# Kernel tuning notes

Measured on AMD Instinct MI355X. Metric: run time of the kernel, lower is better.

The kernel has to match this reference:

```python
import jax, jax.numpy as jnp
import numpy as np

# fp4 e2m1 positive value grid and midpoints between adjacent grid values
_GRID = jnp.array([0.0, 0.5, 1.0, 1.5, 2.0, 3.0, 4.0, 6.0], dtype=jnp.float32)
_MIDS = jnp.array([0.25, 0.75, 1.25, 1.75, 2.5, 3.5, 5.0], dtype=jnp.float32)
BLOCK = 32               # MX block size
E8M0_BIAS = 127
F32_MIN_NORMAL = float(2.0 ** -126)
F4_E2M1_MAX_POW2 = 2     # log2 of largest power-of-two <= 6.0 -> 4.0


def _quantize_fp4(a):
    """Round-to-nearest-even onto the signed e2m1 grid."""
    mag = jnp.clip(jnp.abs(a), 0.0, 6.0)
    idx = jnp.searchsorted(_MIDS, mag, side='left')  # ties round down
    mids_pad = jnp.concatenate([_MIDS, jnp.array([-1.0], jnp.float32)])
    tie = mag == mids_pad[idx]
    idx = jnp.where(tie & (idx % 2 == 1), idx + 1, idx)  # ties-to-even mantissa
    return _GRID[idx] * jnp.where(a < 0, -1.0, 1.0)


def _floor_log2(m):
    """Exact floor(log2(m)) for m > 0, with corrections for fp rounding of log2."""
    e = jnp.floor(jnp.log2(m))
    e = jnp.where(jnp.exp2(e) > m, e - 1.0, e)
    e = jnp.where(jnp.exp2(e + 1.0) <= m, e + 1.0, e)
    return e


def _qdq_mxfp4(x):
    """Quantize-dequantize x to MX fp4_e2m1, block 32, FLOOR scale mode (to_mx + to_dtype)."""
    shp = x.shape
    xb = x.reshape(-1, BLOCK)
    max_abs = jnp.max(jnp.abs(xb), axis=1)
    eps = F32_MIN_NORMAL * (max_abs == 0).astype(jnp.float32)
    pow2 = _floor_log2(max_abs + eps)
    e_unb = jnp.clip(pow2 - F4_E2M1_MAX_POW2, -float(E8M0_BIAS), float(E8M0_BIAS) + 1.0)
    scale = jnp.maximum(jnp.exp2(e_unb), F32_MIN_NORMAL)  # [nblk]
    q = _quantize_fp4(xb / scale[:, None])
    return (q * scale[:, None]).reshape(shp)


def _dequant_weight(weight_packed, weight_scale, out_f, in_f):
    """Unpack uint8-packed fp4 (low nibble first), apply e8m0 block scales."""
    p = weight_packed.astype(jnp.int32)
    low = p & 0xF
    high = (p >> 4) & 0xF
    nib = jnp.stack([low, high], axis=-1).reshape(out_f, in_f)  # interleave low,high
    vals = _GRID[nib & 7] * jnp.where((nib & 8) > 0, -1.0, 1.0)
    s = jnp.exp2(weight_scale.astype(jnp.float32) - E8M0_BIAS)  # get_fp_scale(e8m0)
    return (vals.reshape(-1, BLOCK) * s[:, None]).reshape(out_f, in_f)


def setup_inputs() -> dict:
    key = jax.random.key(0)
    k1, k2, k3 = jax.random.split(key, 3)
    M, IN, OUT = 4096, 4096, 4096
    x = jax.random.normal(k1, (M, IN), dtype=jnp.float32)
    weight_packed = jax.random.randint(k2, (OUT, IN // 2), 0, 256, dtype=jnp.int32)
    weight_scale = jax.random.randint(k3, (OUT * IN // BLOCK,), 0, 135, dtype=jnp.int32)
    return {"x": x, "weight_packed": weight_packed, "weight_scale": weight_scale}


def reference(x, weight_packed, weight_scale):
    out_f = weight_packed.shape[0]
    in_f = weight_packed.shape[1] * 2
    xq = _qdq_mxfp4(x)                                       # qdq_mxfp4(x)
    w_dq = _dequant_weight(weight_packed, weight_scale, out_f, in_f)
    return xq @ w_dq.T                                       # matmul(x, w_dq.t())
```

## Files before the change

kernel.cpp:

```cpp
#include <hip/hip_runtime.h>
#include <stdint.h>

typedef __attribute__((ext_vector_type(4)))  int   intx4;
typedef __attribute__((ext_vector_type(8)))  int   intx8;
typedef __attribute__((ext_vector_type(16))) float floatx16;

#define GLL16(gp, lp)                                                               \
    __builtin_amdgcn_global_load_lds((const __attribute__((address_space(1))) unsigned int*)(gp), \
                                     (__attribute__((address_space(3))) unsigned int*)(lp), 16, 0, 0)
#define GLL4(gp, lp)                                                                \
    __builtin_amdgcn_global_load_lds((const __attribute__((address_space(1))) unsigned int*)(gp), \
                                     (__attribute__((address_space(3))) unsigned int*)(lp), 4, 0, 0)

__device__ __forceinline__ uint32_t enc1(float xv, float inv) {
    float a = fminf(fabsf(xv) * inv, 6.0f);
    int e;
    if (a < 2.0f)      e = (int)rintf(a + a);
    else if (a < 4.0f) e = (int)rintf(a) + 2;
    else               e = (int)rintf(a * 0.5f) + 4;
    return (uint32_t)e | ((__float_as_uint(xv) >> 28) & 8u);
}

__global__ __launch_bounds__(256) void quant_x_kernel(const float* __restrict__ x,
                                                      uint32_t* __restrict__ xq,
                                                      uint8_t* __restrict__ xs_t,
                                                      int M, int K) {
    int t = blockIdx.x * 256 + threadIdx.x;
    int kbpr = K >> 5;
    int m = t / kbpr;
    int kb = t - m * kbpr;
    const float4* src = (const float4*)(x + (size_t)m * K + (size_t)kb * 32);
    float4 v[8];
#pragma unroll
    for (int i = 0; i < 8; ++i) v[i] = src[i];
    float mx = 0.f;
#pragma unroll
    for (int i = 0; i < 8; ++i)
        mx = fmaxf(mx, fmaxf(fmaxf(fabsf(v[i].x), fabsf(v[i].y)),
                             fmaxf(fabsf(v[i].z), fabsf(v[i].w))));
    unsigned ef = __float_as_uint(mx) >> 23;
    unsigned code = (ef < 3u) ? 1u : (ef - 2u);
    float inv = __uint_as_float((254u - code) << 23);

    uint32_t w[4];
#pragma unroll
    for (int d = 0; d < 4; ++d) {
        float4 va = v[2 * d], vb = v[2 * d + 1];
        w[d] =  enc1(va.x, inv)        | (enc1(va.y, inv) << 4)
             | (enc1(va.z, inv) << 8)  | (enc1(va.w, inv) << 12)
             | (enc1(vb.x, inv) << 16) | (enc1(vb.y, inv) << 20)
             | (enc1(vb.z, inv) << 24) | (enc1(vb.w, inv) << 28);
    }
    ((uint4*)xq)[t] = make_uint4(w[0], w[1], w[2], w[3]);
    xs_t[(size_t)kb * M + m] = (uint8_t)code;
}

__global__ __launch_bounds__(256) void tscale_kernel(const int* __restrict__ wsc,
                                                     uint8_t* __restrict__ ws_t,
                                                     int N, int kbpr) {
    int t = blockIdx.x * 256 + threadIdx.x;
    int n = t / kbpr;
    int kb = t - n * kbpr;
    ws_t[(size_t)kb * N + n] = (uint8_t)wsc[t];
}

__global__ __launch_bounds__(256) void repack_w_kernel(const int* __restrict__ wp,
                                                       uint32_t* __restrict__ wrep,
                                                       int n4) {
    int t = blockIdx.x * 256 + threadIdx.x;
    if (t >= n4) return;
    int4 p = ((const int4*)wp)[t];
    wrep[t] = (uint32_t)(p.x & 0xFF) | ((uint32_t)(p.y & 0xFF) << 8)
            | ((uint32_t)(p.z & 0xFF) << 16) | ((uint32_t)(p.w & 0xFF) << 24);
}

__global__ __launch_bounds__(256) void gemm_mx_kernel(const uint8_t* __restrict__ Apk,
                                                      const uint8_t* __restrict__ Bpk,
                                                      const uint8_t* __restrict__ AsT,
                                                      const uint8_t* __restrict__ BsT,
                                                      float* __restrict__ C,
                                                      int M, int N, int K) {
    __shared__ __align__(16) uint8_t sA[8192];
    __shared__ __align__(16) uint8_t sB[8192];
    __shared__ __align__(16) uint8_t sAs[512];
    __shared__ __align__(16) uint8_t sBs[512];

    const int tid = threadIdx.x;
    const int bm0 = blockIdx.y << 7;
    const int bn0 = blockIdx.x << 7;
    const int wave = tid >> 6;
    const int lane = tid & 63;
    const int wm = (wave >> 1) << 6;
    const int wn = (wave & 1) << 6;
    const int row = lane & 31;
    const int h = lane >> 5;
    const int Kb = K >> 1;

    const int s0 = tid, s1 = tid + 256;
    const int r0 = s0 >> 2, p0 = (s0 & 3) ^ (r0 & 3);
    const int r1 = s1 >> 2, p1 = (s1 & 3) ^ (r1 & 3);
    const uint8_t* Ag0 = Apk + (size_t)(bm0 + r0) * Kb + p0 * 16;
    const uint8_t* Ag1 = Apk + (size_t)(bm0 + r1) * Kb + p1 * 16;
    const uint8_t* Bg0 = Bpk + (size_t)(bn0 + r0) * Kb + p0 * 16;
    const uint8_t* Bg1 = Bpk + (size_t)(bn0 + r1) * Kb + p1 * 16;

    const int st = tid & 127;
    const int sj = st >> 5, si = st & 31;
    const uint8_t* Sg = (tid < 128) ? (AsT + (size_t)sj * M + bm0 + si * 4)
                                    : (BsT + (size_t)sj * N + bn0 + si * 4);
    uint8_t* Sl = (tid < 128) ? (sAs + st * 4) : (sBs + st * 4);
    const size_t sAdv = (size_t)4 * (size_t)((tid < 128) ? M : N);

    floatx16 acc[2][2];
#pragma unroll
    for (int a = 0; a < 2; ++a)
#pragma unroll
        for (int b = 0; b < 2; ++b)
#pragma unroll
            for (int r = 0; r < 16; ++r) acc[a][b][r] = 0.f;

    const int nchunk = K >> 7;
    for (int c = 0; c < nchunk; ++c) {
        __syncthreads();
        const size_t koff = (size_t)c << 6;
        GLL16(Ag0 + koff, sA + s0 * 16);
        GLL16(Ag1 + koff, sA + s1 * 16);
        GLL16(Bg0 + koff, sB + s0 * 16);
        GLL16(Bg1 + koff, sB + s1 * 16);
        GLL4(Sg + (size_t)c * sAdv, Sl);
        __syncthreads();

#pragma unroll
        for (int s = 0; s < 2; ++s) {
            intx4 a4[2], b4[2];
            int sa[2], sb[2];
            const int kp = 2 * s + h;
#pragma unroll
            for (int mt = 0; mt < 2; ++mt) {
                const int lr = wm + mt * 32 + row;
                a4[mt] = *(const intx4*)(sA + lr * 64 + ((kp ^ (lr & 3)) << 4));
                sa[mt] = sAs[kp * 128 + lr];
            }
#pragma unroll
            for (int nt = 0; nt < 2; ++nt) {
                const int lr = wn + nt * 32 + row;
                b4[nt] = *(const intx4*)(sB + lr * 64 + ((kp ^ (lr & 3)) << 4));
                sb[nt] = sBs[kp * 128 + lr];
            }
#pragma unroll
            for (int mt = 0; mt < 2; ++mt)
#pragma unroll
                for (int nt = 0; nt < 2; ++nt) {
                    intx8 a8 = {a4[mt][0], a4[mt][1], a4[mt][2], a4[mt][3], 0, 0, 0, 0};
                    intx8 b8 = {b4[nt][0], b4[nt][1], b4[nt][2], b4[nt][3], 0, 0, 0, 0};
                    acc[mt][nt] = __builtin_amdgcn_mfma_scale_f32_32x32x64_f8f6f4(
                        a8, b8, acc[mt][nt], 4, 4, 0, sa[mt], 0, sb[nt]);
                }
        }
    }

#pragma unroll
    for (int mt = 0; mt < 2; ++mt)
#pragma unroll
        for (int nt = 0; nt < 2; ++nt) {
            const int col = bn0 + wn + nt * 32 + row;
#pragma unroll
            for (int g = 0; g < 4; ++g) {
                const int rw = bm0 + wm + mt * 32 + 8 * g + 4 * h;
#pragma unroll
                for (int q = 0; q < 4; ++q)
                    C[(size_t)(rw + q) * N + col] = acc[mt][nt][4 * g + q];
            }
        }
}

extern "C" void kernel_launch(void* const* d_in, const int* in_sizes, int n_in,
                              void* d_out, int out_size, void* d_ws, size_t ws_size,
                              hipStream_t stream) {
    const float* x = (const float*)d_in[0];
    const int* wp = (const int*)d_in[1];
    const int* wsc = (const int*)d_in[2];
    float* out = (float*)d_out;

    const int K = 4096;
    const int M = in_sizes[0] / K;
    const int N = (in_sizes[1] * 2) / K;
    const int kbpr = K / 32;
    const int npack = N * K / 2;

    uint32_t* xq   = (uint32_t*)d_ws;
    uint8_t*  xs   = (uint8_t*)d_ws + (size_t)M * K / 2;
    uint8_t*  wst  = xs + (size_t)M * kbpr;
    uint32_t* wrep = (uint32_t*)(wst + (size_t)N * kbpr);

    quant_x_kernel<<<(M * kbpr) / 256, 256, 0, stream>>>(x, xq, xs, M, K);
    tscale_kernel<<<(N * kbpr) / 256, 256, 0, stream>>>(wsc, wst, N, kbpr);
    repack_w_kernel<<<(npack / 4 + 255) / 256, 256, 0, stream>>>(wp, wrep, npack / 4);

    dim3 grid(N / 128, M / 128);
    gemm_mx_kernel<<<grid, 256, 0, stream>>>((const uint8_t*)xq, (const uint8_t*)wrep,
                                             xs, wst, out, M, N, K);
}
```

Baseline: 204.2 us.

## Double-buffer GEMM LDS loads, row-major scales, fuse weight prep kernels

The GEMM main loop now uses two LDS buffers: the next K-chunk is issued with global_load_lds while the current one is computed, and explicit vmcnt waits plus barriers replace the two __syncthreads per chunk. MFMA sections are wrapped in s_setprio. Scales are stored row-major so each thread loads four consecutive scale bytes as one word, which removes the transposing scale kernel. The weight repack and scale packing are fused into one launch, and x quantization is remapped to one float4 per thread with a shuffle-based block max, which gives coalesced small writes at the cost of more threads. Doubling LDS use may lower occupancy.

```diff
diff --git a/kernel.cpp b/kernel.cpp
--- a/kernel.cpp
+++ b/kernel.cpp
@@ -23,67 +23,50 @@
 
 __global__ __launch_bounds__(256) void quant_x_kernel(const float* __restrict__ x,
                                                       uint32_t* __restrict__ xq,
-                                                      uint8_t* __restrict__ xs_t,
-                                                      int M, int K) {
-    int t = blockIdx.x * 256 + threadIdx.x;
-    int kbpr = K >> 5;
-    int m = t / kbpr;
-    int kb = t - m * kbpr;
-    const float4* src = (const float4*)(x + (size_t)m * K + (size_t)kb * 32);
-    float4 v[8];
-#pragma unroll
-    for (int i = 0; i < 8; ++i) v[i] = src[i];
-    float mx = 0.f;
-#pragma unroll
-    for (int i = 0; i < 8; ++i)
-        mx = fmaxf(mx, fmaxf(fmaxf(fabsf(v[i].x), fabsf(v[i].y)),
-                             fmaxf(fabsf(v[i].z), fabsf(v[i].w))));
-    unsigned ef = __float_as_uint(mx) >> 23;
-    unsigned code = (ef < 3u) ? 1u : (ef - 2u);
-    float inv = __uint_as_float((254u - code) << 23);
-
-    uint32_t w[4];
-#pragma unroll
-    for (int d = 0; d < 4; ++d) {
-        float4 va = v[2 * d], vb = v[2 * d + 1];
-        w[d] =  enc1(va.x, inv)        | (enc1(va.y, inv) << 4)
-             | (enc1(va.z, inv) << 8)  | (enc1(va.w, inv) << 12)
-             | (enc1(vb.x, inv) << 16) | (enc1(vb.y, inv) << 20)
-             | (enc1(vb.z, inv) << 24) | (enc1(vb.w, inv) << 28);
+                                                      uint8_t* __restrict__ xs) {
+    const int gl = blockIdx.x * 256 + threadIdx.x;
+    const float4 v = ((const float4*)x)[gl];
+    float m = fmaxf(fmaxf(fabsf(v.x), fabsf(v.y)), fmaxf(fabsf(v.z), fabsf(v.w)));
+    m = fmaxf(m, __shfl_xor(m, 1));
+    m = fmaxf(m, __shfl_xor(m, 2));
+    m = fmaxf(m, __shfl_xor(m, 4));
+    const unsigned ef = __float_as_uint(m) >> 23;
+    const unsigned code = (ef < 3u) ? 1u : (ef - 2u);
+    const float inv = __uint_as_float((254u - code) << 23);
+    const uint32_t p = enc1(v.x, inv)        | (enc1(v.y, inv) << 4)
+                     | (enc1(v.z, inv) << 8) | (enc1(v.w, inv) << 12);
+    ((uint16_t*)xq)[gl] = (uint16_t)p;
+    if ((gl & 7) == 0) xs[gl >> 3] = (uint8_t)code;
+}
+
+__global__ __launch_bounds__(256) void repack_kernel(const int* __restrict__ wp,
+                                                     uint32_t* __restrict__ wrep,
+                                                     int n4w,
+                                                     const int* __restrict__ wsc,
+                                                     uint32_t* __restrict__ ws,
+                                                     int n4s) {
+    const int t = blockIdx.x * 256 + threadIdx.x;
+    if (t < n4w) {
+        const int4 p = ((const int4*)wp)[t];
+        wrep[t] = (uint32_t)(p.x & 0xFF) | ((uint32_t)(p.y & 0xFF) << 8)
+                | ((uint32_t)(p.z & 0xFF) << 16) | ((uint32_t)(p.w & 0xFF) << 24);
+    } else if (t - n4w < n4s) {
+        const int i = t - n4w;
+        const int4 p = ((const int4*)wsc)[i];
+        ws[i] = (uint32_t)(p.x & 0xFF) | ((uint32_t)(p.y & 0xFF) << 8)
+              | ((uint32_t)(p.z & 0xFF) << 16) | ((uint32_t)(p.w & 0xFF) << 24);
     }
-    ((uint4*)xq)[t] = make_uint4(w[0], w[1], w[2], w[3]);
-    xs_t[(size_t)kb * M + m] = (uint8_t)code;
-}
-
-__global__ __launch_bounds__(256) void tscale_kernel(const int* __restrict__ wsc,
-                                                     uint8_t* __restrict__ ws_t,
-                                                     int N, int kbpr) {
-    int t = blockIdx.x * 256 + threadIdx.x;
-    int n = t / kbpr;
-    int kb = t - n * kbpr;
-    ws_t[(size_t)kb * N + n] = (uint8_t)wsc[t];
-}
-
-__global__ __launch_bounds__(256) void repack_w_kernel(const int* __restrict__ wp,
-                                                       uint32_t* __restrict__ wrep,
-                                                       int n4) {
-    int t = blockIdx.x * 256 + threadIdx.x;
-    if (t >= n4) return;
-    int4 p = ((const int4*)wp)[t];
-    wrep[t] = (uint32_t)(p.x & 0xFF) | ((uint32_t)(p.y & 0xFF) << 8)
-            | ((uint32_t)(p.z & 0xFF) << 16) | ((uint32_t)(p.w & 0xFF) << 24);
 }
 
 __global__ __launch_bounds__(256) void gemm_mx_kernel(const uint8_t* __restrict__ Apk,
                                                       const uint8_t* __restrict__ Bpk,
-                                                      const uint8_t* __restrict__ AsT,
-                                                      const uint8_t* __restrict__ BsT,
+                                                      const uint8_t* __restrict__ As,
+                                                      const uint8_t* __restrict__ Bs,
                                                       float* __restrict__ C,
                                                       int M, int N, int K) {
-    __shared__ __align__(16) uint8_t sA[8192];
-    __shared__ __align__(16) uint8_t sB[8192];
-    __shared__ __align__(16) uint8_t sAs[512];
-    __shared__ __align__(16) uint8_t sBs[512];
+    __shared__ __align__(16) uint8_t sA[2][8192];
+    __shared__ __align__(16) uint8_t sB[2][8192];
+    __shared__ __align__(16) uint8_t sS[2][1024];
 
     const int tid = threadIdx.x;
     const int bm0 = blockIdx.y << 7;
@@ -95,6 +78,7 @@
     const int row = lane & 31;
     const int h = lane >> 5;
     const int Kb = K >> 1;
+    const int kbpr = K >> 5;
 
     const int s0 = tid, s1 = tid + 256;
     const int r0 = s0 >> 2, p0 = (s0 & 3) ^ (r0 & 3);
@@ -104,12 +88,10 @@
     const uint8_t* Bg0 = Bpk + (size_t)(bn0 + r0) * Kb + p0 * 16;
     const uint8_t* Bg1 = Bpk + (size_t)(bn0 + r1) * Kb + p1 * 16;
 
-    const int st = tid & 127;
-    const int sj = st >> 5, si = st & 31;
-    const uint8_t* Sg = (tid < 128) ? (AsT + (size_t)sj * M + bm0 + si * 4)
-                                    : (BsT + (size_t)sj * N + bn0 + si * 4);
-    uint8_t* Sl = (tid < 128) ? (sAs + st * 4) : (sBs + st * 4);
-    const size_t sAdv = (size_t)4 * (size_t)((tid < 128) ? M : N);
+    const int srow = tid & 127;
+    const uint8_t* Sg = (tid < 128) ? (As + (size_t)(bm0 + srow) * kbpr)
+                                    : (Bs + (size_t)(bn0 + srow) * kbpr);
+    const int sldoff = ((tid < 128) ? 0 : 512) + srow * 4;
 
     floatx16 acc[2][2];
 #pragma unroll
@@ -120,33 +102,36 @@
             for (int r = 0; r < 16; ++r) acc[a][b][r] = 0.f;
 
     const int nchunk = K >> 7;
-    for (int c = 0; c < nchunk; ++c) {
-        __syncthreads();
+
+    auto STAGE = [&](int bf, int c) {
         const size_t koff = (size_t)c << 6;
-        GLL16(Ag0 + koff, sA + s0 * 16);
-        GLL16(Ag1 + koff, sA + s1 * 16);
-        GLL16(Bg0 + koff, sB + s0 * 16);
-        GLL16(Bg1 + koff, sB + s1 * 16);
-        GLL4(Sg + (size_t)c * sAdv, Sl);
-        __syncthreads();
-
+        GLL16(Ag0 + koff, &sA[bf][s0 * 16]);
+        GLL16(Ag1 + koff, &sA[bf][s1 * 16]);
+        GLL16(Bg0 + koff, &sB[bf][s0 * 16]);
+        GLL16(Bg1 + koff, &sB[bf][s1 * 16]);
+        GLL4(Sg + (size_t)c * 4, &sS[bf][sldoff]);
+    };
+
+    const int ar0 = wm + row, ar1 = wm + 32 + row;
+    const int br0 = wn + row, br1 = wn + 32 + row;
+
+    auto COMPUTE = [&](int bf) {
+        const uint32_t saw0 = *(const uint32_t*)&sS[bf][ar0 * 4];
+        const uint32_t saw1 = *(const uint32_t*)&sS[bf][ar1 * 4];
+        const uint32_t sbw0 = *(const uint32_t*)&sS[bf][512 + br0 * 4];
+        const uint32_t sbw1 = *(const uint32_t*)&sS[bf][512 + br1 * 4];
 #pragma unroll
         for (int s = 0; s < 2; ++s) {
+            const int kp = 2 * s + h;
+            const int sh = kp * 8;
             intx4 a4[2], b4[2];
-            int sa[2], sb[2];
-            const int kp = 2 * s + h;
-#pragma unroll
-            for (int mt = 0; mt < 2; ++mt) {
-                const int lr = wm + mt * 32 + row;
-                a4[mt] = *(const intx4*)(sA + lr * 64 + ((kp ^ (lr & 3)) << 4));
-                sa[mt] = sAs[kp * 128 + lr];
-            }
-#pragma unroll
-            for (int nt = 0; nt < 2; ++nt) {
-                const int lr = wn + nt * 32 + row;
-                b4[nt] = *(const intx4*)(sB + lr * 64 + ((kp ^ (lr & 3)) << 4));
-                sb[nt] = sBs[kp * 128 + lr];
-            }
+            a4[0] = *(const intx4*)&sA[bf][ar0 * 64 + ((kp ^ (ar0 & 3)) << 4)];
+            a4[1] = *(const intx4*)&sA[bf][ar1 * 64 + ((kp ^ (ar1 & 3)) << 4)];
+            b4[0] = *(const intx4*)&sB[bf][br0 * 64 + ((kp ^ (br0 & 3)) << 4)];
+            b4[1] = *(const intx4*)&sB[bf][br1 * 64 + ((kp ^ (br1 & 3)) << 4)];
+            const int sa[2] = { (int)((saw0 >> sh) & 0xFF), (int)((saw1 >> sh) & 0xFF) };
+            const int sb[2] = { (int)((sbw0 >> sh) & 0xFF), (int)((sbw1 >> sh) & 0xFF) };
+            __builtin_amdgcn_s_setprio(1);
 #pragma unroll
             for (int mt = 0; mt < 2; ++mt)
 #pragma unroll
@@ -156,8 +141,22 @@
                     acc[mt][nt] = __builtin_amdgcn_mfma_scale_f32_32x32x64_f8f6f4(
                         a8, b8, acc[mt][nt], 4, 4, 0, sa[mt], 0, sb[nt]);
                 }
+            __builtin_amdgcn_s_setprio(0);
         }
+    };
+
+    STAGE(0, 0);
+    for (int c = 0; c < nchunk - 1; ++c) {
+        const int bf = c & 1;
+        STAGE(bf ^ 1, c + 1);
+        asm volatile("s_waitcnt vmcnt(5)" ::: "memory");
+        __builtin_amdgcn_s_barrier();
+        COMPUTE(bf);
+        __builtin_amdgcn_s_barrier();
     }
+    asm volatile("s_waitcnt vmcnt(0)" ::: "memory");
+    __builtin_amdgcn_s_barrier();
+    COMPUTE((nchunk - 1) & 1);
 
 #pragma unroll
     for (int mt = 0; mt < 2; ++mt)
@@ -190,14 +189,17 @@
 
     uint32_t* xq   = (uint32_t*)d_ws;
     uint8_t*  xs   = (uint8_t*)d_ws + (size_t)M * K / 2;
-    uint8_t*  wst  = xs + (size_t)M * kbpr;
-    uint32_t* wrep = (uint32_t*)(wst + (size_t)N * kbpr);
-
-    quant_x_kernel<<<(M * kbpr) / 256, 256, 0, stream>>>(x, xq, xs, M, K);
-    tscale_kernel<<<(N * kbpr) / 256, 256, 0, stream>>>(wsc, wst, N, kbpr);
-    repack_w_kernel<<<(npack / 4 + 255) / 256, 256, 0, stream>>>(wp, wrep, npack / 4);
+    uint8_t*  ws   = xs + (size_t)M * kbpr;
+    uint32_t* wrep = (uint32_t*)(ws + (size_t)N * kbpr);
+
+    const int n4w = npack / 4;
+    const int n4s = (N * kbpr) / 4;
+
+    quant_x_kernel<<<(M * K / 4) / 256, 256, 0, stream>>>(x, xq, xs);
+    repack_kernel<<<(n4w + n4s + 255) / 256, 256, 0, stream>>>(wp, wrep, n4w,
+                                                               wsc, (uint32_t*)ws, n4s);
 
     dim3 grid(N / 128, M / 128);
     gemm_mx_kernel<<<grid, 256, 0, stream>>>((const uint8_t*)xq, (const uint8_t*)wrep,
-                                             xs, wst, out, M, N, K);
-}
+                                             xs, ws, out, M, N, K);
+}
```

Result: slower. 210.7 us (+3.2%).
